# Kernel tuning notes

Measured on AMD Instinct MI355X. Metric: run time of the kernel, lower is better.

The kernel has to match this reference:

```python
import jax, jax.numpy as jnp
import numpy as np

DIM_X, H1, H2 = 1024, 2048, 512
SL, SU = 8192, 16384
K_TRIES = 8  # vectorized stand-in for the per-sample rejection-sampling while-loop


def setup_inputs() -> dict:
    key = jax.random.key(0)
    ks = jax.random.split(key, 10)
    s = 0.02
    return {
        "X_l": jax.random.normal(ks[0], (SL, DIM_X), jnp.float32),
        "y_l": jax.random.normal(ks[1], (SL,), jnp.float32),
        "X_u": jax.random.normal(ks[2], (SU, DIM_X), jnp.float32),
        "y_u": jax.random.normal(ks[3], (SU,), jnp.float32),
        "W1": jax.random.normal(ks[4], (DIM_X, H1), jnp.float32) * s,
        "b1": jnp.zeros((H1,), jnp.float32),
        "W2": jax.random.normal(ks[5], (H1, H2), jnp.float32) * s,
        "b2": jnp.zeros((H2,), jnp.float32),
        "W3": jax.random.normal(ks[6], (H2, 1), jnp.float32) * s,
        "b3": jnp.zeros((1,), jnp.float32),
    }


def _sample_pairs(key, y_l, size_u):
    """For each unlabeled sample, draw a labeled pair (a, b) with a != b and
    y_l[a] != y_l[b] (mirrors torch.randperm + rejection loop). K candidate
    draws per sample; first valid candidate is taken (valid w.h.p. for
    continuous y_l)."""
    size_l = y_l.shape[0]
    ka, kb = jax.random.split(key)
    ia = jax.random.randint(ka, (size_u, K_TRIES), 0, size_l)  # [SU, K]
    ib = jax.random.randint(kb, (size_u, K_TRIES), 0, size_l)
    valid = (ia != ib) & (y_l[ia] != y_l[ib])
    first = jnp.argmax(valid, axis=1)  # first valid candidate per row
    a = jnp.take_along_axis(ia, first[:, None], axis=1)[:, 0]
    b = jnp.take_along_axis(ib, first[:, None], axis=1)[:, 0]
    return a, b


def reference(X_l, y_l, X_u, y_u, W1, b1, W2, b2, W3, b3):
    def encode(x):
        h = jax.nn.relu(x @ W1 + b1)
        return jax.nn.relu(h @ W2 + b2)

    feat_l = encode(X_l)          # [SL, H2]
    feat_u = encode(X_u)          # [SU, H2]
    y_hat = feat_l @ W3 + b3      # [SL, 1]

    a, b = _sample_pairs(jax.random.key(42), y_l, X_u.shape[0])
    k = (y_u - y_l[b]) / (y_l[a] - y_l[b])            # [SU]
    feat_comb = k[:, None] * feat_l[a] + (1.0 - k)[:, None] * feat_l[b]
    return feat_u, feat_comb, y_hat
```

## Files before the change

kernel.cpp:

```cpp
#include <hip/hip_runtime.h>
#include <stdint.h>

#define SLAB 8192
#define SUNL 16384
#define DIMX 1024
#define HID1 2048
#define HID2 512
#define KTRIES 8
#define MTOT (SLAB + SUNL)

typedef __attribute__((ext_vector_type(8))) short bf16x8;
typedef __attribute__((ext_vector_type(4))) float f32x4;
typedef __attribute__((ext_vector_type(16))) float f32x16;

__device__ __forceinline__ unsigned short f2bf(float f) {
  union { float f; uint32_t u; } c; c.f = f;
  return (unsigned short)((c.u + 0x7fffu + ((c.u >> 16) & 1u)) >> 16);
}

__device__ __forceinline__ void async16(const void* g, void* l) {
  __builtin_amdgcn_global_load_lds(
      (const __attribute__((address_space(1))) unsigned int*)g,
      (__attribute__((address_space(3))) unsigned int*)l,
      16, 0, 0);
}

struct U2 { uint32_t x, y; };

__device__ __forceinline__ U2 threefry(uint32_t k0, uint32_t k1, uint32_t x0, uint32_t x1) {
  uint32_t ks2 = k0 ^ k1 ^ 0x1BD11BDAu;
  x0 += k0; x1 += k1;
#define TF_R(r) { x0 += x1; x1 = (x1 << (r)) | (x1 >> (32 - (r))); x1 ^= x0; }
  TF_R(13) TF_R(15) TF_R(26) TF_R(6)
  x0 += k1; x1 += ks2 + 1u;
  TF_R(17) TF_R(29) TF_R(16) TF_R(24)
  x0 += ks2; x1 += k0 + 2u;
  TF_R(13) TF_R(15) TF_R(26) TF_R(6)
  x0 += k0; x1 += k1 + 3u;
  TF_R(17) TF_R(29) TF_R(16) TF_R(24)
  x0 += k1; x1 += ks2 + 4u;
  TF_R(13) TF_R(15) TF_R(26) TF_R(6)
  x0 += ks2; x1 += k0 + 5u;
#undef TF_R
  return {x0, x1};
}

#define XL_BLOCKS (SLAB * DIMX / 4 / 256)
#define CAST_BLOCKS (MTOT * DIMX / 4 / 256)
#define T1_NBX (HID1 / 32)
#define T1_BLOCKS ((HID1 / 32) * (DIMX / 32))
#define T2_NBX (HID2 / 32)
#define T2_BLOCKS ((HID2 / 32) * (HID1 / 32))
#define PAIR_BLOCKS (SUNL / 256)
#define PREP_BLOCKS (CAST_BLOCKS + T1_BLOCKS + T2_BLOCKS + PAIR_BLOCKS)

__global__ __launch_bounds__(256) void prep_kernel(
    const float* __restrict__ Xl, const float* __restrict__ Xu,
    const float* __restrict__ W1, const float* __restrict__ W2,
    const float* __restrict__ y_l, const float* __restrict__ y_u,
    unsigned short* __restrict__ X_bf, unsigned short* __restrict__ W1T,
    unsigned short* __restrict__ W2T,
    int* __restrict__ ia, int* __restrict__ ib, float* __restrict__ kv)
{
  __shared__ float t[32][33];
  int b = blockIdx.x;
  int tid = threadIdx.x;

  if (b < CAST_BLOCKS) {
    const float* src; size_t i, doff;
    if (b < XL_BLOCKS) { src = Xl; i = (size_t)b * 256 + tid; doff = 0; }
    else { src = Xu; i = (size_t)(b - XL_BLOCKS) * 256 + tid; doff = (size_t)SLAB * DIMX / 4; }
    float4 v = ((const float4*)src)[i];
    ushort4 o;
    o.x = f2bf(v.x); o.y = f2bf(v.y); o.z = f2bf(v.z); o.w = f2bf(v.w);
    ((ushort4*)X_bf)[doff + i] = o;
  } else if (b < CAST_BLOCKS + T1_BLOCKS + T2_BLOCKS) {
    const float* W; unsigned short* WT; int K, N, bx, by;
    if (b < CAST_BLOCKS + T1_BLOCKS) {
      int tb = b - CAST_BLOCKS;
      W = W1; WT = W1T; K = DIMX; N = HID1; bx = tb % T1_NBX; by = tb / T1_NBX;
    } else {
      int tb = b - CAST_BLOCKS - T1_BLOCKS;
      W = W2; WT = W2T; K = HID1; N = HID2; bx = tb % T2_NBX; by = tb / T2_NBX;
    }
    int k0 = by * 32, n0 = bx * 32;
    int tx = tid & 31, ty = tid >> 5;
#pragma unroll
    for (int i = 0; i < 32; i += 8)
      t[ty + i][tx] = W[(size_t)(k0 + ty + i) * N + n0 + tx];
    __syncthreads();
#pragma unroll
    for (int i = 0; i < 32; i += 8)
      WT[(size_t)(n0 + ty + i) * K + k0 + tx] = f2bf(t[tx][ty + i]);
  } else {
    int r = (b - CAST_BLOCKS - T1_BLOCKS - T2_BLOCKS) * 256 + tid;
    U2 ka  = threefry(0u, 42u, 0u, 0u);
    U2 kb  = threefry(0u, 42u, 0u, 1u);
    U2 k2a = threefry(ka.x, ka.y, 0u, 1u);
    U2 k2b = threefry(kb.x, kb.y, 0u, 1u);
    int iav[KTRIES], ibv[KTRIES];
#pragma unroll
    for (int c = 0; c < KTRIES; ++c) {
      uint32_t tt = (uint32_t)(r * KTRIES + c);
      U2 oa = threefry(k2a.x, k2a.y, 0u, tt);
      U2 ob = threefry(k2b.x, k2b.y, 0u, tt);
      iav[c] = (int)((oa.x ^ oa.y) & (SLAB - 1));
      ibv[c] = (int)((ob.x ^ ob.y) & (SLAB - 1));
    }
    int a = iav[0], bb2 = ibv[0];
#pragma unroll
    for (int c = 0; c < KTRIES; ++c) {
      if (iav[c] != ibv[c] && y_l[iav[c]] != y_l[ibv[c]]) { a = iav[c]; bb2 = ibv[c]; break; }
    }
    float ya = y_l[a], yb = y_l[bb2];
    ia[r] = a; ib[r] = bb2; kv[r] = (y_u[r] - yb) / (ya - yb);
  }
}

#define GROUP_M 8

template<int OUT_BF16, int RELU>
__global__ __launch_bounds__(256) void gemm_bt_mfma(
    const unsigned short* __restrict__ A,
    const unsigned short* __restrict__ Bt,
    const float* __restrict__ bias,
    void* __restrict__ C0, void* __restrict__ C1, int Msplit,
    int M, int N, int K)
{
  __shared__ unsigned short As[128 * 32];
  __shared__ unsigned short Bs[128 * 32];

  const int tid  = threadIdx.x;
  const int wave = tid >> 6;
  const int lane = tid & 63;

  const int nbx = N / 128;
  const int gsize = nbx * GROUP_M;
  const int grp = blockIdx.x / gsize, within = blockIdx.x % gsize;
  const int m0 = (grp * GROUP_M + (within % GROUP_M)) * 128;
  const int n0 = (within / GROUP_M) * 128;

  const int wm = (wave >> 1) * 64;
  const int wn = (wave & 1) * 64;

  const int srow  = wave * 32 + (lane >> 2);
  const int gchunk = ((lane & 3) - (srow >> 1)) & 3;
  const unsigned short* gA = A  + (size_t)(m0 + srow) * K + gchunk * 8;
  const unsigned short* gB = Bt + (size_t)(n0 + srow) * K + gchunk * 8;
  unsigned short* lA = As + wave * 32 * 32;
  unsigned short* lB = Bs + wave * 32 * 32;

  const int r31 = lane & 31;
  const int cHalf = lane >> 5;

  f32x16 acc[2][2] = {};

  for (int k0 = 0; k0 < K; k0 += 32) {
    async16(gA + k0,                  lA);
    async16(gA + k0 + (size_t)16 * K, lA + 16 * 32);
    async16(gB + k0,                  lB);
    async16(gB + k0 + (size_t)16 * K, lB + 16 * 32);
    __syncthreads();

    bf16x8 ar[2][2], br[2][2];
#pragma unroll
    for (int i = 0; i < 2; ++i) {
      int rowA = wm + i * 32 + r31;
      int rowB = wn + i * 32 + r31;
#pragma unroll
      for (int kk = 0; kk < 2; ++kk) {
        int c = kk * 2 + cHalf;
        ar[i][kk] = *(const bf16x8*)(As + rowA * 32 + ((c + (rowA >> 1)) & 3) * 8);
        br[i][kk] = *(const bf16x8*)(Bs + rowB * 32 + ((c + (rowB >> 1)) & 3) * 8);
      }
    }
#pragma unroll
    for (int kk = 0; kk < 2; ++kk)
#pragma unroll
      for (int i = 0; i < 2; ++i)
#pragma unroll
        for (int j = 0; j < 2; ++j)
          acc[i][j] = __builtin_amdgcn_mfma_f32_32x32x16_bf16(ar[i][kk], br[j][kk], acc[i][j], 0, 0, 0);
    __syncthreads();
  }

  void* Cb = (m0 < Msplit) ? C0 : C1;
  const int mbase = ((m0 < Msplit) ? m0 : (m0 - Msplit)) + wm;
  const int ccolBase = n0 + wn + (lane & 31);
  const int crowHi = (lane >> 5) * 4;
#pragma unroll
  for (int j = 0; j < 2; ++j) {
    float bv = bias[ccolBase + j * 32];
#pragma unroll
    for (int i = 0; i < 2; ++i) {
#pragma unroll
      for (int reg = 0; reg < 16; ++reg) {
        int row = (reg & 3) + 8 * (reg >> 2) + crowHi;
        float v = acc[i][j][reg] + bv;
        if (RELU) v = fmaxf(v, 0.0f);
        size_t idx = (size_t)(mbase + i * 32 + row) * N + ccolBase + j * 32;
        if (OUT_BF16) ((unsigned short*)Cb)[idx] = f2bf(v);
        else          ((float*)Cb)[idx] = v;
      }
    }
  }
}

#define COMB_BLOCKS (SUNL / 2)
#define YHAT_BLOCKS (SLAB / 4)
#define POST_BLOCKS (COMB_BLOCKS + YHAT_BLOCKS)

__global__ __launch_bounds__(256) void post_kernel(
    const float* __restrict__ feat_l, const float* __restrict__ W3,
    const float* __restrict__ b3, const int* __restrict__ ia,
    const int* __restrict__ ib, const float* __restrict__ kv,
    float* __restrict__ out_comb, float* __restrict__ out_yhat)
{
  int b = blockIdx.x;
  if (b < COMB_BLOCKS) {
    int row = b * 2 + (threadIdx.x >> 7);
    int c = (threadIdx.x & 127) << 2;
    float k = kv[row];
    float km1 = 1.0f - k;
    float4 fa = *(const float4*)(feat_l + (size_t)ia[row] * HID2 + c);
    float4 fb = *(const float4*)(feat_l + (size_t)ib[row] * HID2 + c);
    float4 o;
    o.x = k * fa.x + km1 * fb.x;
    o.y = k * fa.y + km1 * fb.y;
    o.z = k * fa.z + km1 * fb.z;
    o.w = k * fa.w + km1 * fb.w;
    *(float4*)(out_comb + (size_t)row * HID2 + c) = o;
  } else {
    int wave = threadIdx.x >> 6;
    int lane = threadIdx.x & 63;
    int row = (b - COMB_BLOCKS) * 4 + wave;
    const float* f = feat_l + (size_t)row * HID2;
    float s = 0.f;
#pragma unroll
    for (int j = 0; j < HID2 / 64; ++j) s = fmaf(f[lane + j * 64], W3[lane + j * 64], s);
#pragma unroll
    for (int off = 32; off; off >>= 1) s += __shfl_down(s, off);
    if (lane == 0) out_yhat[row] = s + b3[0];
  }
}

extern "C" void kernel_launch(void* const* d_in, const int* in_sizes, int n_in,
                              void* d_out, int out_size, void* d_ws, size_t ws_size,
                              hipStream_t stream)
{
  const float* X_l = (const float*)d_in[0];
  const float* y_l = (const float*)d_in[1];
  const float* X_u = (const float*)d_in[2];
  const float* y_u = (const float*)d_in[3];
  const float* W1  = (const float*)d_in[4];
  const float* b1  = (const float*)d_in[5];
  const float* W2  = (const float*)d_in[6];
  const float* b2  = (const float*)d_in[7];
  const float* W3  = (const float*)d_in[8];
  const float* b3  = (const float*)d_in[9];

  float* out_featu = (float*)d_out;
  float* out_comb  = out_featu + (size_t)SUNL * HID2;
  float* out_yhat  = out_comb + (size_t)SUNL * HID2;

  unsigned short* X_bf  = (unsigned short*)d_ws;
  unsigned short* W1T   = X_bf + (size_t)MTOT * DIMX;
  unsigned short* W2T   = W1T + (size_t)HID1 * DIMX;
  unsigned short* H_bf  = W2T + (size_t)HID2 * HID1;
  float* feat_l = (float*)(H_bf + (size_t)MTOT * HID1);
  int*   ai = (int*)(feat_l + (size_t)SLAB * HID2);
  int*   bi = ai + SUNL;
  float* kv = (float*)(bi + SUNL);

  dim3 blk(256);

  prep_kernel<<<dim3(PREP_BLOCKS), blk, 0, stream>>>(
      X_l, X_u, W1, W2, y_l, y_u, X_bf, W1T, W2T, ai, bi, kv);

  gemm_bt_mfma<1, 1><<<dim3((HID1 / 128) * (MTOT / 128)), blk, 0, stream>>>(
      X_bf, W1T, b1, H_bf, H_bf, MTOT * 2 , MTOT, HID1, DIMX);

  gemm_bt_mfma<0, 1><<<dim3((HID2 / 128) * (MTOT / 128)), blk, 0, stream>>>(
      H_bf, W2T, b2, feat_l, out_featu, SLAB, MTOT, HID2, HID1);

  post_kernel<<<dim3(POST_BLOCKS), blk, 0, stream>>>(
      feat_l, W3, b3, ai, bi, kv, out_comb, out_yhat);
}
```

Before: 391.0 us.

## Use 16x16x32 MFMA with 64-wide K tiles and 8-slot swizzled LDS

The GEMM now stages 128x64 K-tiles, twice the previous depth, which halves the number of barrier pairs per K. It also switches from 32x32x16 MFMAs to 16x16x32 MFMAs with a 4x4 accumulator grid per wave, using a new 8-slot XOR-style LDS swizzle and a matching epilogue layout. The aim is to cut synchronisation overhead and improve LDS access patterns. In exchange it doubles LDS use per block, which may reduce occupancy, and relies on the new swizzle being conflict-free.

```diff
diff --git a/kernel.cpp b/kernel.cpp
--- a/kernel.cpp
+++ b/kernel.cpp
@@ -11,7 +11,6 @@
 
 typedef __attribute__((ext_vector_type(8))) short bf16x8;
 typedef __attribute__((ext_vector_type(4))) float f32x4;
-typedef __attribute__((ext_vector_type(16))) float f32x16;
 
 __device__ __forceinline__ unsigned short f2bf(float f) {
   union { float f; uint32_t u; } c; c.f = f;
@@ -127,8 +126,8 @@
     void* __restrict__ C0, void* __restrict__ C1, int Msplit,
     int M, int N, int K)
 {
-  __shared__ unsigned short As[128 * 32];
-  __shared__ unsigned short Bs[128 * 32];
+  __shared__ unsigned short As[128 * 64];
+  __shared__ unsigned short Bs[128 * 64];
 
   const int tid  = threadIdx.x;
   const int wave = tid >> 6;
@@ -143,62 +142,61 @@
   const int wm = (wave >> 1) * 64;
   const int wn = (wave & 1) * 64;
 
-  const int srow  = wave * 32 + (lane >> 2);
-  const int gchunk = ((lane & 3) - (srow >> 1)) & 3;
+  const int srow = wave * 32 + (lane >> 3);
+  const int gchunk = ((lane & 7) - (lane >> 3)) & 7;
   const unsigned short* gA = A  + (size_t)(m0 + srow) * K + gchunk * 8;
   const unsigned short* gB = Bt + (size_t)(n0 + srow) * K + gchunk * 8;
-  unsigned short* lA = As + wave * 32 * 32;
-  unsigned short* lB = Bs + wave * 32 * 32;
-
-  const int r31 = lane & 31;
-  const int cHalf = lane >> 5;
-
-  f32x16 acc[2][2] = {};
-
-  for (int k0 = 0; k0 < K; k0 += 32) {
-    async16(gA + k0,                  lA);
-    async16(gA + k0 + (size_t)16 * K, lA + 16 * 32);
-    async16(gB + k0,                  lB);
-    async16(gB + k0 + (size_t)16 * K, lB + 16 * 32);
+  unsigned short* lA = As + wave * 32 * 64;
+  unsigned short* lB = Bs + wave * 32 * 64;
+
+  const int fr = lane & 15;
+  const int q  = lane >> 4;
+
+  f32x4 acc[4][4] = {};
+
+  for (int k0 = 0; k0 < K; k0 += 64) {
+#pragma unroll
+    for (int c = 0; c < 4; ++c) {
+      async16(gA + k0 + (size_t)(c * 8) * K, lA + c * 8 * 64);
+      async16(gB + k0 + (size_t)(c * 8) * K, lB + c * 8 * 64);
+    }
     __syncthreads();
 
-    bf16x8 ar[2][2], br[2][2];
-#pragma unroll
-    for (int i = 0; i < 2; ++i) {
-      int rowA = wm + i * 32 + r31;
-      int rowB = wn + i * 32 + r31;
-#pragma unroll
-      for (int kk = 0; kk < 2; ++kk) {
-        int c = kk * 2 + cHalf;
-        ar[i][kk] = *(const bf16x8*)(As + rowA * 32 + ((c + (rowA >> 1)) & 3) * 8);
-        br[i][kk] = *(const bf16x8*)(Bs + rowB * 32 + ((c + (rowB >> 1)) & 3) * 8);
+#pragma unroll
+    for (int s = 0; s < 2; ++s) {
+      bf16x8 ar[4], br[4];
+#pragma unroll
+      for (int i = 0; i < 4; ++i) {
+        int rowA = wm + i * 16 + fr;
+        int rowB = wn + i * 16 + fr;
+        int slotA = ((s * 4 + q + rowA) & 7) * 8;
+        int slotB = ((s * 4 + q + rowB) & 7) * 8;
+        ar[i] = *(const bf16x8*)(As + rowA * 64 + slotA);
+        br[i] = *(const bf16x8*)(Bs + rowB * 64 + slotB);
       }
-    }
-#pragma unroll
-    for (int kk = 0; kk < 2; ++kk)
-#pragma unroll
-      for (int i = 0; i < 2; ++i)
-#pragma unroll
-        for (int j = 0; j < 2; ++j)
-          acc[i][j] = __builtin_amdgcn_mfma_f32_32x32x16_bf16(ar[i][kk], br[j][kk], acc[i][j], 0, 0, 0);
+#pragma unroll
+      for (int i = 0; i < 4; ++i)
+#pragma unroll
+        for (int j = 0; j < 4; ++j)
+          acc[i][j] = __builtin_amdgcn_mfma_f32_16x16x32_bf16(ar[i], br[j], acc[i][j], 0, 0, 0);
+    }
     __syncthreads();
   }
 
   void* Cb = (m0 < Msplit) ? C0 : C1;
-  const int mbase = ((m0 < Msplit) ? m0 : (m0 - Msplit)) + wm;
-  const int ccolBase = n0 + wn + (lane & 31);
-  const int crowHi = (lane >> 5) * 4;
-#pragma unroll
-  for (int j = 0; j < 2; ++j) {
-    float bv = bias[ccolBase + j * 32];
-#pragma unroll
-    for (int i = 0; i < 2; ++i) {
-#pragma unroll
-      for (int reg = 0; reg < 16; ++reg) {
-        int row = (reg & 3) + 8 * (reg >> 2) + crowHi;
-        float v = acc[i][j][reg] + bv;
+  const int mbase = (m0 < Msplit) ? m0 : (m0 - Msplit);
+  const int crow = mbase + wm + (lane >> 4) * 4;
+  const int ccol = n0 + wn + (lane & 15);
+#pragma unroll
+  for (int j = 0; j < 4; ++j) {
+    float bv = bias[ccol + j * 16];
+#pragma unroll
+    for (int i = 0; i < 4; ++i) {
+#pragma unroll
+      for (int r = 0; r < 4; ++r) {
+        float v = acc[i][j][r] + bv;
         if (RELU) v = fmaxf(v, 0.0f);
-        size_t idx = (size_t)(mbase + i * 32 + row) * N + ccolBase + j * 32;
+        size_t idx = (size_t)(crow + i * 16 + r) * N + ccol + j * 16;
         if (OUT_BF16) ((unsigned short*)Cb)[idx] = f2bf(v);
         else          ((float*)Cb)[idx] = v;
       }
```

Result: no change. 383.8 us (-1.8%).
